# Optimization experiments

Measured on AMD Instinct MI355X. Metric: run time of the kernel, lower is better.

The kernel has to match this reference:

```python
import jax, jax.numpy as jnp
import numpy as np

L, D, V, BS, H, HD, DL = 12, 768, 50257, 1024, 12, 64, 256
B, T = 2, 1024
EPS = 1e-5


def _ln(x, w, b):
    m = jnp.mean(x, axis=-1, keepdims=True)
    v = jnp.mean((x - m) ** 2, axis=-1, keepdims=True)
    return (x - m) * jax.lax.rsqrt(v + EPS) * w + b


def _rope_tables(t_len):
    inv_freq = 1.0 / (10000.0 ** (jnp.arange(0, HD, 2, dtype=jnp.float32) / HD))
    t = jnp.arange(t_len, dtype=jnp.float32)
    freqs = jnp.outer(t, inv_freq)  # [T, HD/2]
    return jnp.cos(freqs), jnp.sin(freqs)


def _apply_rope(x, cos, sin):
    # x: [B, H, T, HD]; cos/sin: [T, HD/2]
    c = jnp.concatenate([cos, cos], axis=-1)[None, None]
    s = jnp.concatenate([sin, sin], axis=-1)[None, None]
    x1, x2 = jnp.split(x, 2, axis=-1)
    rot = jnp.concatenate([-x2, x1], axis=-1)
    return x * c + rot * s


def setup_inputs() -> dict:
    key = jax.random.key(0)
    ks = jax.random.split(key, 16)
    std = 0.02
    n = lambda k, shape: jax.random.normal(k, shape, dtype=jnp.float32) * std
    return {
        'idx': jax.random.randint(ks[0], (B, T), 0, V),
        'wte': n(ks[1], (V, D)),
        'wpe': n(ks[2], (BS, D)),
        'ln1_w': jnp.ones((L, D)), 'ln1_b': jnp.zeros((L, D)),
        'wq_w': n(ks[3], (L, D, H * HD)), 'wq_b': jnp.zeros((L, H * HD)),
        'kva_w': n(ks[4], (L, D, DL)), 'kva_b': jnp.zeros((L, DL)),
        'kvb_w': n(ks[5], (L, DL, 2 * H * HD)), 'kvb_b': jnp.zeros((L, 2 * H * HD)),
        'out_w': n(ks[6], (L, H * HD, D)), 'out_b': jnp.zeros((L, D)),
        'ln2_w': jnp.ones((L, D)), 'ln2_b': jnp.zeros((L, D)),
        'fc_w': n(ks[7], (L, D, 4 * D)), 'fc_b': jnp.zeros((L, 4 * D)),
        'proj_w': n(ks[8], (L, 4 * D, D)), 'proj_b': jnp.zeros((L, D)),
        'lnf_w': jnp.ones((D,)), 'lnf_b': jnp.zeros((D,)),
    }


def _forward(idx, wte, wpe, ln1_w, ln1_b, wq_w, wq_b, kva_w, kva_b, kvb_w, kvb_b,
             out_w, out_b, ln2_w, ln2_b, fc_w, fc_b, proj_w, proj_b, lnf_w, lnf_b):
    b, t = idx.shape
    x = wte[idx] + wpe[:t][None]  # [B,T,D]
    cos, sin = _rope_tables(t)
    scale = 1.0 / np.sqrt(HD)
    causal = jnp.tril(jnp.ones((t, t), dtype=bool))
    for l in range(L):
        h = _ln(x, ln1_w[l], ln1_b[l])
        q = (h @ wq_w[l] + wq_b[l]).reshape(b, t, H, HD).transpose(0, 2, 1, 3)
        kv_latent = h @ kva_w[l] + kva_b[l]  # [B,T,DL] (the cacheable latent)
        kv = (kv_latent @ kvb_w[l] + kvb_b[l]).reshape(b, t, 2, H, HD)
        kv = kv.transpose(2, 0, 3, 1, 4)  # [2,B,H,T,HD]
        k, v = kv[0], kv[1]
        q = _apply_rope(q, cos, sin)
        k = _apply_rope(k, cos, sin)
        scores = jnp.einsum('bhtd,bhsd->bhts', q, k) * scale
        scores = jnp.where(causal[None, None], scores, -jnp.inf)
        probs = jax.nn.softmax(scores, axis=-1)
        attn = jnp.einsum('bhts,bhsd->bhtd', probs, v)
        attn = attn.transpose(0, 2, 1, 3).reshape(b, t, H * HD)
        x = x + attn @ out_w[l] + out_b[l]
        h2 = _ln(x, ln2_w[l], ln2_b[l])
        mlp = jax.nn.gelu(h2 @ fc_w[l] + fc_b[l], approximate=False) @ proj_w[l] + proj_b[l]
        x = x + mlp
    x = _ln(x, lnf_w, lnf_b)
    logits = x @ wte.T  # tied lm_head
    return logits


def reference(idx, wte, wpe, ln1_w, ln1_b, wq_w, wq_b, kva_w, kva_b, kvb_w, kvb_b,
              out_w, out_b, ln2_w, ln2_b, fc_w, fc_b, proj_w, proj_b, lnf_w, lnf_b):
    return _forward(idx, wte, wpe, ln1_w, ln1_b, wq_w, wq_b, kva_w, kva_b, kvb_w,
                    kvb_b, out_w, out_b, ln2_w, ln2_b, fc_w, fc_b, proj_w, proj_b,
                    lnf_w, lnf_b)
```

## Files before the change

kernel.cpp:

```cpp
#include <hip/hip_runtime.h>
#include <cstdint>
#include <cstddef>


typedef unsigned short ushortT;
typedef __bf16 bf16x8 __attribute__((ext_vector_type(8)));
typedef float f32x4 __attribute__((ext_vector_type(4)));

#define NHEAD 12
#define T_SEQ 1024

__device__ __forceinline__ float bf2f(unsigned short u) {
    union { unsigned int i; float f; } v; v.i = ((unsigned int)u) << 16; return v.f;
}
__device__ __forceinline__ unsigned short f2bf(float f) {
    union { float f; unsigned int i; } v; v.f = f;
    unsigned int r = v.i + 0x7fffu + ((v.i >> 16) & 1u);
    return (unsigned short)(r >> 16);
}
__device__ __forceinline__ unsigned int pack2(float a, float b) {
    return (unsigned int)f2bf(a) | ((unsigned int)f2bf(b) << 16);
}
__device__ __forceinline__ void gload_lds16(const void* g, void* l) {
    __builtin_amdgcn_global_load_lds((__attribute__((address_space(1))) void*)g,
                                     (__attribute__((address_space(3))) void*)l, 16, 0, 0);
}
template <int N>
__device__ __forceinline__ void wait_vmcnt() {
    if constexpr (N == 8)      asm volatile("s_waitcnt vmcnt(8)" ::: "memory");
    else if constexpr (N == 6) asm volatile("s_waitcnt vmcnt(6)" ::: "memory");
    else if constexpr (N == 5) asm volatile("s_waitcnt vmcnt(5)" ::: "memory");
    else if constexpr (N == 4) asm volatile("s_waitcnt vmcnt(4)" ::: "memory");
    else if constexpr (N == 3) asm volatile("s_waitcnt vmcnt(3)" ::: "memory");
    else                       asm volatile("s_waitcnt vmcnt(0)" ::: "memory");
}

__global__ __launch_bounds__(256) void transpose_cvt_kernel(
    const float* __restrict__ in, ushortT* __restrict__ outp,
    int K, int N, int outRowOff, size_t outLS) {
    __shared__ float tile[32][33];
    const int tid = threadIdx.x;
    const int n0 = blockIdx.x * 32, k0 = blockIdx.y * 32;
    const float* src = in + (size_t)blockIdx.z * K * N;
    {
        const int r = tid >> 3, cg = tid & 7;
        float4 v = *(const float4*)(src + (size_t)(k0 + r) * N + n0 + cg * 4);
        tile[r][cg * 4 + 0] = v.x; tile[r][cg * 4 + 1] = v.y;
        tile[r][cg * 4 + 2] = v.z; tile[r][cg * 4 + 3] = v.w;
    }
    __syncthreads();
    {
        const int nr = tid >> 3, kg = tid & 7;
        ushort4 o;
        o.x = f2bf(tile[kg * 4 + 0][nr]);
        o.y = f2bf(tile[kg * 4 + 1][nr]);
        o.z = f2bf(tile[kg * 4 + 2][nr]);
        o.w = f2bf(tile[kg * 4 + 3][nr]);
        ushortT* dst = outp + (size_t)blockIdx.z * outLS;
        *(ushort4*)(dst + (size_t)(outRowOff + n0 + nr) * K + k0 + kg * 4) = o;
    }
}

__global__ void cvt_wte_kernel(const float* __restrict__ in, ushortT* __restrict__ outp) {
    size_t i4 = (size_t)blockIdx.x * 256 + threadIdx.x;
    ushort4 o;
    if (i4 < 9649344) {
        float4 v = ((const float4*)in)[i4];
        o.x = f2bf(v.x); o.y = f2bf(v.y); o.z = f2bf(v.z); o.w = f2bf(v.w);
    } else { o.x = 0; o.y = 0; o.z = 0; o.w = 0; }
    ((ushort4*)outp)[i4] = o;
}

__global__ void embed_kernel(const int* __restrict__ idx, const float* __restrict__ wte,
                             const float* __restrict__ wpe, float* __restrict__ x) {
    int i = blockIdx.x * 256 + threadIdx.x;
    int row = i / 768, d = i - row * 768;
    int t = row & 1023;
    x[i] = wte[(size_t)idx[row] * 768 + d] + wpe[(size_t)t * 768 + d];
}

__global__ void rope_tables_kernel(float* __restrict__ cosT, float* __restrict__ sinT) {
    int i = blockIdx.x * 256 + threadIdx.x;
    int t = i >> 5, f = i & 31;
    float invf = exp2f(-(float)f * (13.287712379549449f / 32.0f));
    float ang = (float)t * invf;
    cosT[i] = cosf(ang);
    sinT[i] = sinf(ang);
}

__global__ __launch_bounds__(256) void ln_kernel(const float* __restrict__ x,
                                                 const float* __restrict__ wg,
                                                 const float* __restrict__ bg,
                                                 ushortT* __restrict__ outp) {
    const int row = blockIdx.x, tid = threadIdx.x;
    const float* xr = x + (size_t)row * 768;
    float v0 = xr[tid], v1 = xr[tid + 256], v2 = xr[tid + 512];
    float s = v0 + v1 + v2;
    float ss = v0 * v0 + v1 * v1 + v2 * v2;
#pragma unroll
    for (int off = 32; off >= 1; off >>= 1) {
        s += __shfl_xor(s, off);
        ss += __shfl_xor(ss, off);
    }
    __shared__ float sb[4], ssb[4];
    if ((tid & 63) == 0) { sb[tid >> 6] = s; ssb[tid >> 6] = ss; }
    __syncthreads();
    float S = sb[0] + sb[1] + sb[2] + sb[3];
    float SS = ssb[0] + ssb[1] + ssb[2] + ssb[3];
    const float mean = S * (1.0f / 768.0f);
    float var = SS * (1.0f / 768.0f) - mean * mean;
    const float rs = rsqrtf(var + 1e-5f);
    ushortT* orow = outp + (size_t)row * 768;
    orow[tid]       = f2bf((v0 - mean) * rs * wg[tid]       + bg[tid]);
    orow[tid + 256] = f2bf((v1 - mean) * rs * wg[tid + 256] + bg[tid + 256]);
    orow[tid + 512] = f2bf((v2 - mean) * rs * wg[tid + 512] + bg[tid + 512]);
}

template <int NP>
__global__ __launch_bounds__(256) void reduce_ln_kernel(
    float* __restrict__ x, const float* __restrict__ part,
    const float* __restrict__ bias,
    const float* __restrict__ wg, const float* __restrict__ bg,
    ushortT* __restrict__ outp) {
    const int row = blockIdx.x, tid = threadIdx.x;
    const size_t base = (size_t)row * 768;
    float4 v = {0.f, 0.f, 0.f, 0.f};
    if (tid < 192) {
        v = *(const float4*)(x + base + tid * 4);
        const float4 b4 = *(const float4*)(bias + tid * 4);
        v.x += b4.x; v.y += b4.y; v.z += b4.z; v.w += b4.w;
#pragma unroll
        for (int p = 0; p < NP; ++p) {
            const float4 pv = *(const float4*)(part + (size_t)p * 1572864 + base + tid * 4);
            v.x += pv.x; v.y += pv.y; v.z += pv.z; v.w += pv.w;
        }
        *(float4*)(x + base + tid * 4) = v;
    }
    float s = v.x + v.y + v.z + v.w;
    float ss = v.x * v.x + v.y * v.y + v.z * v.z + v.w * v.w;
#pragma unroll
    for (int off = 32; off >= 1; off >>= 1) {
        s += __shfl_xor(s, off);
        ss += __shfl_xor(ss, off);
    }
    __shared__ float sb[4], ssb[4];
    if ((tid & 63) == 0) { sb[tid >> 6] = s; ssb[tid >> 6] = ss; }
    __syncthreads();
    const float S = sb[0] + sb[1] + sb[2] + sb[3];
    const float SS = ssb[0] + ssb[1] + ssb[2] + ssb[3];
    const float mean = S * (1.0f / 768.0f);
    const float var = SS * (1.0f / 768.0f) - mean * mean;
    const float rs = rsqrtf(var + 1e-5f);
    if (tid < 192) {
        const float4 w4 = *(const float4*)(wg + tid * 4);
        const float4 g4 = *(const float4*)(bg + tid * 4);
        ushort4 o;
        o.x = f2bf((v.x - mean) * rs * w4.x + g4.x);
        o.y = f2bf((v.y - mean) * rs * w4.y + g4.y);
        o.z = f2bf((v.z - mean) * rs * w4.z + g4.z);
        o.w = f2bf((v.w - mean) * rs * w4.w + g4.w);
        *(ushort4*)(outp + base + tid * 4) = o;
    }
}

template <int BM, int NF, int NTHR, bool ROPE, bool PARTIAL = false>
__global__ __launch_bounds__(NTHR) void gemmT(
    const ushortT* __restrict__ A, int lda,
    const ushortT* __restrict__ Bt, int ldb,
    int K, int CS, int Nstore,
    const float* __restrict__ bias0, const float* __restrict__ bias1,
    ushortT* __restrict__ outB0, int ld0,
    ushortT* __restrict__ outB1, int ld1, int mode1,
    const float* __restrict__ resid, float* __restrict__ outF, int ldF,
    int act, const float* __restrict__ cosT, const float* __restrict__ sinT) {
    constexpr int WC = (NTHR == 512) ? 4 : 2;
    constexpr int WMR = BM / 2;
    constexpr int MF = WMR / 16;
    constexpr int NFh = NF / WC;
    constexpr int WNh = NFh * 16;
    constexpr int ABYTES = BM * 128;
    constexpr int BBYTES = NF * 2048;
    constexpr int BUFB = ABYTES + BBYTES;
    constexpr int A_LOADS = (BM * 8) / NTHR;
    constexpr int B_LOADS = (NF * 128) / NTHR;
    constexpr int S = A_LOADS + B_LOADS;
    __shared__ __align__(16) char lds[2 * BUFB];
    const int tid = threadIdx.x;
    const int w = tid >> 6, lane = tid & 63;
    const int wm = w / WC, wn = w % WC;
    const int gx = gridDim.x;
    const int nwg = gx * gridDim.y;
    const int flat = blockIdx.x + gx * blockIdx.y;
    const int xcd = flat & 7, loc = flat >> 3;
    const int qq = nwg >> 3, rr_ = nwg & 7;
    const int swz = (xcd < rr_ ? xcd * (qq + 1) : rr_ * (qq + 1) + (xcd - rr_) * qq) + loc;
    const int m0 = (swz % gx) * BM, n0 = (swz / gx) * NF * 16;
    const int fr = lane & 15, kg = lane >> 4;
    const size_t ldaB = (size_t)lda * 2, ldbB = (size_t)ldb * 2;
    int koff = 0;
    if constexpr (PARTIAL) koff = blockIdx.z * K;
    const char* Ab = (const char*)A + (size_t)koff * 2;
    const char* Bb = (const char*)Bt + (size_t)koff * 2;
    float* outFz = outF;
    if constexpr (PARTIAL) outFz = outF + (size_t)blockIdx.z * 2048 * (size_t)ldF;
    f32x4 acc[MF][NFh] = {};

    auto stage = [&](int buf, int t) {
        const size_t ktB = (size_t)t << 7;
        char* As_ = lds + buf * BUFB;
        char* Bs_ = As_ + ABYTES;
#pragma unroll
        for (int jj = 0; jj < A_LOADS; ++jj) {
            const int i = tid + jj * NTHR;
            const int r = i >> 3, c = i & 7, cc = c ^ (r & 7);
            gload_lds16(Ab + (size_t)(m0 + r) * ldaB + ktB + cc * 16, As_ + i * 16);
        }
#pragma unroll
        for (int jj = 0; jj < B_LOADS; ++jj) {
            const int i = tid + jj * NTHR;
            const int r = i >> 3, c = i & 7, cc = c ^ (r & 7);
            gload_lds16(Bb + (size_t)(n0 + r) * ldbB + ktB + cc * 16, Bs_ + i * 16);
        }
    };

    const int nk = K >> 6;
    stage(0, 0);
    if (nk > 1) { stage(1, 1); wait_vmcnt<S>(); }
    else        { wait_vmcnt<0>(); }
    __builtin_amdgcn_s_barrier();

    for (int t = 0; t < nk; ++t) {
        const int cur = t & 1;
        const char* As_ = lds + cur * BUFB;
        const char* Bs_ = As_ + ABYTES;
        bf16x8 af[MF][2], bfr[NFh][2];
#pragma unroll
        for (int mf = 0; mf < MF; ++mf) {
            const int row = wm * WMR + mf * 16 + fr;
#pragma unroll
            for (int ks = 0; ks < 2; ++ks)
                af[mf][ks] = *(const bf16x8*)(As_ + row * 128 + (((ks * 4 + kg) ^ (row & 7)) << 4));
        }
#pragma unroll
        for (int nf = 0; nf < NFh; ++nf) {
            const int row = wn * WNh + nf * 16 + fr;
#pragma unroll
            for (int ks = 0; ks < 2; ++ks)
                bfr[nf][ks] = *(const bf16x8*)(Bs_ + row * 128 + (((ks * 4 + kg) ^ (row & 7)) << 4));
        }
        if (t + 2 < nk) {
            asm volatile("s_waitcnt lgkmcnt(0)" ::: "memory");
            __builtin_amdgcn_s_barrier();
            stage(cur, t + 2);
        }
#pragma unroll
        for (int ks = 0; ks < 2; ++ks)
#pragma unroll
            for (int nf = 0; nf < NFh; ++nf)
#pragma unroll
                for (int mf = 0; mf < MF; ++mf)
                    acc[mf][nf] = __builtin_amdgcn_mfma_f32_16x16x32_bf16(
                        af[mf][ks], bfr[nf][ks], acc[mf][nf], 0, 0, 0);
        if (t + 1 < nk) {
            if (t + 2 < nk) wait_vmcnt<S>();
            else            wait_vmcnt<0>();
            __builtin_amdgcn_s_barrier();
        }
    }

    if constexpr (ROPE) {
        float vv[MF][4][4];
#pragma unroll
        for (int mf = 0; mf < MF; ++mf)
#pragma unroll
            for (int nf = 0; nf < 4; ++nf) {
                const int gcol = n0 + wn * 64 + nf * 16 + fr;
                float bv = (gcol < CS) ? (bias0 ? bias0[gcol] : 0.0f)
                                       : (bias1 ? bias1[gcol - CS] : 0.0f);
#pragma unroll
                for (int j = 0; j < 4; ++j) vv[mf][nf][j] = acc[mf][nf][j] + bv;
            }
        if (n0 + wn * 64 < 768) {
#pragma unroll
            for (int mf = 0; mf < MF; ++mf)
#pragma unroll
                for (int j = 0; j < 4; ++j) {
                    const int grow = m0 + wm * WMR + mf * 16 + kg * 4 + j;
                    const int t = grow & 1023;
                    const float c0 = cosT[t * 32 + fr],      s0 = sinT[t * 32 + fr];
                    const float c1 = cosT[t * 32 + 16 + fr], s1 = sinT[t * 32 + 16 + fr];
                    float x1 = vv[mf][0][j], x2 = vv[mf][2][j];
                    vv[mf][0][j] = x1 * c0 - x2 * s0;
                    vv[mf][2][j] = x2 * c0 + x1 * s0;
                    float y1 = vv[mf][1][j], y2 = vv[mf][3][j];
                    vv[mf][1][j] = y1 * c1 - y2 * s1;
                    vv[mf][3][j] = y2 * c1 + y1 * s1;
                }
        }
#pragma unroll
        for (int mf = 0; mf < MF; ++mf)
#pragma unroll
            for (int nf = 0; nf < 4; ++nf) {
                const int gcol = n0 + wn * 64 + nf * 16 + fr;
                if (gcol >= Nstore) continue;
#pragma unroll
                for (int j = 0; j < 4; ++j) {
                    const int grow = m0 + wm * WMR + mf * 16 + kg * 4 + j;
                    const float v = vv[mf][nf][j];
                    if (gcol < CS) {
                        if (outB0) outB0[(size_t)grow * ld0 + gcol] = f2bf(v);
                    } else if (outB1) {
                        if (mode1 == 0) {
                            outB1[(size_t)grow * ld1 + gcol - CS] = f2bf(v);
                        } else {
                            const int bb = grow >> 10, tt = grow & 1023;
                            const int hd = gcol - CS;
                            outB1[((size_t)((bb * 12 + (hd >> 6)) * 64 + (hd & 63)) << 10) + tt] = f2bf(v);
                        }
                    }
                }
            }
    } else {
#pragma unroll
        for (int mf = 0; mf < MF; ++mf) {
#pragma unroll
            for (int nf = 0; nf < NFh; ++nf) {
                const int gcol = n0 + wn * WNh + nf * 16 + fr;
                if (gcol >= Nstore) continue;
                float bv = 0.0f;
                if (gcol < CS) { if (bias0) bv = bias0[gcol]; }
                else           { if (bias1) bv = bias1[gcol - CS]; }
#pragma unroll
                for (int j = 0; j < 4; ++j) {
                    const int grow = m0 + wm * WMR + mf * 16 + kg * 4 + j;
                    float v = acc[mf][nf][j] + bv;
                    if (resid) v += resid[(size_t)grow * ldF + gcol];
                    if (act) v = 0.5f * v * (1.0f + erff(v * 0.70710678118654752f));
                    if (outFz) outFz[(size_t)grow * ldF + gcol] = v;
                    if (gcol < CS) {
                        if (outB0) outB0[(size_t)grow * ld0 + gcol] = f2bf(v);
                    } else if (outB1) {
                        if (mode1 == 0) {
                            outB1[(size_t)grow * ld1 + gcol - CS] = f2bf(v);
                        } else {
                            const int bb = grow >> 10, tt = grow & 1023;
                            const int hd = gcol - CS;
                            outB1[((size_t)((bb * 12 + (hd >> 6)) * 64 + (hd & 63)) << 10) + tt] = f2bf(v);
                        }
                    }
                }
            }
        }
    }
}

#define FC_PHASE(SLOT, MB, STAGE_STMT, TAILWAIT)                               \
    {                                                                          \
        bf16x8 af[2][2];                                                       \
        _Pragma("unroll") for (int m = 0; m < 2; ++m)                          \
        _Pragma("unroll") for (int ks = 0; ks < 2; ++ks) {                     \
            const int row = wm * 64 + (MB + m) * 16 + fr;                      \
            af[m][ks] = *(const bf16x8*)(lds + (SLOT) * 16384 + row * 128 +    \
                                         (((ks * 4 + kg) ^ (row & 7)) << 4));  \
        }                                                                      \
        STAGE_STMT;                                                            \
        __builtin_amdgcn_s_barrier();                                          \
        asm volatile("s_waitcnt lgkmcnt(0)" ::: "memory");                     \
        __builtin_amdgcn_sched_barrier(0);                                     \
        __builtin_amdgcn_s_setprio(1);                                         \
        _Pragma("unroll") for (int ks = 0; ks < 2; ++ks)                       \
        _Pragma("unroll") for (int nf = 0; nf < NFW; ++nf)                     \
        _Pragma("unroll") for (int m = 0; m < 2; ++m)                          \
            acc[MB + m][nf] = __builtin_amdgcn_mfma_f32_16x16x32_bf16(         \
                af[m][ks], bfr[nf][ks], acc[MB + m][nf], 0, 0, 0);             \
        __builtin_amdgcn_s_setprio(0);                                         \
        TAILWAIT;                                                              \
        __builtin_amdgcn_s_barrier();                                          \
    }

template <int NFW, bool GELU, bool PARTIAL>
__global__ __launch_bounds__(512, 1) void gemm8(
    const ushortT* __restrict__ A, int lda,
    const ushortT* __restrict__ Bt, int ldb,
    const float* __restrict__ bias,
    ushortT* __restrict__ outB, int ldo,
    float* __restrict__ outF) {
    constexpr int BSLOT = NFW * 8192;
    __shared__ __align__(16) char lds[32768 + 2 * BSLOT];
    const int tid = threadIdx.x;
    const int w = tid >> 6, lane = tid & 63;
    const int wm = w >> 2, wn = w & 3;
    const int fr = lane & 15, kg = lane >> 4;
    const int gx = gridDim.x;
    const int nwg = gx * gridDim.y;
    const int flat = blockIdx.x + gx * blockIdx.y;
    const int cpx = nwg >> 3;
    const int swz = (flat & 7) * cpx + (flat >> 3);
    const int m0 = (swz % gx) * 128, n0 = (swz / gx) * (NFW * 64);
    const size_t ldaB = (size_t)lda * 2, ldbB = (size_t)ldb * 2;
    int koff = 0;
    if constexpr (PARTIAL) koff = blockIdx.z * 768;
    const char* Ag = (const char*)A + (size_t)koff * 2;
    const char* Bg = (const char*)Bt + (size_t)koff * 2;
    float* outFz = nullptr;
    if constexpr (PARTIAL) outFz = outF + (size_t)blockIdx.z * 2048 * 768;

    auto stA = [&](int tile) {
        char* dst = lds + (tile & 1) * 16384;
#pragma unroll
        for (int jj = 0; jj < 2; ++jj) {
            const int i = tid + jj * 512;
            const int r = i >> 3, c = i & 7, cc = c ^ (r & 7);
            gload_lds16(Ag + (size_t)(m0 + r) * ldaB + tile * 128 + cc * 16, dst + i * 16);
        }
    };
    auto stB = [&](int tile) {
        char* dst = lds + 32768 + (tile & 1) * BSLOT;
#pragma unroll
        for (int jj = 0; jj < NFW; ++jj) {
            const int i = tid + jj * 512;
            const int r = i >> 3, c = i & 7, cc = c ^ (r & 7);
            gload_lds16(Bg + (size_t)(n0 + r) * ldbB + tile * 128 + cc * 16, dst + i * 16);
        }
    };

    f32x4 acc[4][NFW] = {};
    stA(0); stB(0); stB(1);
    wait_vmcnt<NFW>();
    __builtin_amdgcn_s_barrier();

    const int browB = wn * (NFW * 16);
    for (int i = 0; i < 6; ++i) {
        const int t1 = 2 * i + 1;
        const bool st = (i < 5);
        bf16x8 bfr[NFW][2];
#pragma unroll
        for (int nf = 0; nf < NFW; ++nf)
#pragma unroll
            for (int ks = 0; ks < 2; ++ks) {
                const int row = browB + nf * 16 + fr;
                bfr[nf][ks] = *(const bf16x8*)(lds + 32768 + 0 * BSLOT + row * 128 +
                                               (((ks * 4 + kg) ^ (row & 7)) << 4));
            }
        FC_PHASE(0, 0, stA(t1), )
        FC_PHASE(0, 2, if (st) stB(t1 + 1),
                 if (st) { wait_vmcnt<NFW>(); } else { wait_vmcnt<0>(); }
                 __builtin_amdgcn_sched_barrier(0))
#pragma unroll
        for (int nf = 0; nf < NFW; ++nf)
#pragma unroll
            for (int ks = 0; ks < 2; ++ks) {
                const int row = browB + nf * 16 + fr;
                bfr[nf][ks] = *(const bf16x8*)(lds + 32768 + 1 * BSLOT + row * 128 +
                                               (((ks * 4 + kg) ^ (row & 7)) << 4));
            }
        FC_PHASE(1, 0, if (st) stA(t1 + 1), )
        FC_PHASE(1, 2, if (st) stB(t1 + 2),
                 if (st) { wait_vmcnt<NFW>(); } else { wait_vmcnt<0>(); }
                 __builtin_amdgcn_sched_barrier(0))
    }

#pragma unroll
    for (int mf = 0; mf < 4; ++mf)
#pragma unroll
        for (int nf = 0; nf < NFW; ++nf) {
            const int col = n0 + wn * (NFW * 16) + nf * 16 + fr;
#pragma unroll
            for (int j = 0; j < 4; ++j) {
                const int row = m0 + wm * 64 + mf * 16 + kg * 4 + j;
                if constexpr (PARTIAL) {
                    outFz[(size_t)row * 768 + col] = acc[mf][nf][j];
                } else {
                    float v = acc[mf][nf][j] + bias[col];
                    if constexpr (GELU)
                        v = 0.5f * v * (1.0f + erff(v * 0.70710678118654752f));
                    outB[(size_t)row * ldo + col] = f2bf(v);
                }
            }
        }
}

#define LM_PHASE(SLOT, MB, STAGE_STMT, TAILWAIT)                              \
    {                                                                          \
        bf16x8 af[2][2];                                                       \
        _Pragma("unroll") for (int m = 0; m < 2; ++m)                          \
        _Pragma("unroll") for (int ks = 0; ks < 2; ++ks) {                     \
            const int row = (MB + m) * 16 + fr;                                \
            af[m][ks] = *(const bf16x8*)(Aw + (SLOT) * 32768 + row * 128 +     \
                                         (((ks * 4 + kg) ^ (row & 7)) << 4));  \
        }                                                                      \
        STAGE_STMT;                                                            \
        __builtin_amdgcn_s_barrier();                                          \
        asm volatile("s_waitcnt lgkmcnt(0)" ::: "memory");                     \
        __builtin_amdgcn_sched_barrier(0);                                     \
        __builtin_amdgcn_s_setprio(1);                                         \
        _Pragma("unroll") for (int ks = 0; ks < 2; ++ks)                       \
        _Pragma("unroll") for (int nf = 0; nf < 4; ++nf)                       \
        _Pragma("unroll") for (int m = 0; m < 2; ++m)                          \
            acc[MB + m][nf] = __builtin_amdgcn_mfma_f32_16x16x32_bf16(         \
                af[m][ks], bfr[nf][ks], acc[MB + m][nf], 0, 0, 0);             \
        __builtin_amdgcn_s_setprio(0);                                         \
        TAILWAIT;                                                              \
        __builtin_amdgcn_s_barrier();                                          \
    }

__global__ __launch_bounds__(512, 1) void lmhead8(
    const ushortT* __restrict__ A, const ushortT* __restrict__ Bt,
    float* __restrict__ outF) {
    __shared__ __align__(16) char lds[131072];
    const int tid = threadIdx.x;
    const int w = tid >> 6, lane = tid & 63;
    const int wm = w >> 2, wn = w & 3;
    const int fr = lane & 15, kg = lane >> 4;
    const int flat = blockIdx.x + 8 * blockIdx.y;
    const int swz = (flat & 7) * 197 + (flat >> 3);
    const int m0 = (swz & 7) * 256, n0 = (swz >> 3) * 256;

    const char* Ag = (const char*)A;
    const char* Bg = (const char*)Bt;
    const char* Aw = lds + wm * 16384;
    const char* Bw = lds + 65536 + (wn >> 1) * 16384;
    const int brow0 = (wn & 1) * 64;

    auto stA = [&](int tile, int half) {
        char* dst = lds + (tile & 1) * 32768 + half * 16384;
#pragma unroll
        for (int jj = 0; jj < 2; ++jj) {
            const int i = tid + jj * 512;
            const int r = i >> 3, c = i & 7, cc = c ^ (r & 7);
            gload_lds16(Ag + (size_t)(m0 + half * 128 + r) * 1536 + tile * 128 + cc * 16,
                        dst + i * 16);
        }
    };
    auto stB = [&](int tile, int half) {
        char* dst = lds + 65536 + (tile & 1) * 32768 + half * 16384;
#pragma unroll
        for (int jj = 0; jj < 2; ++jj) {
            const int i = tid + jj * 512;
            const int r = i >> 3, c = i & 7, cc = c ^ (r & 7);
            gload_lds16(Bg + (size_t)(n0 + half * 128 + r) * 1536 + tile * 128 + cc * 16,
                        dst + i * 16);
        }
    };

    f32x4 acc[8][4] = {};
    stA(0, 0); stA(0, 1); stB(0, 0); stB(0, 1); stB(1, 0); stB(1, 1);
    wait_vmcnt<4>();
    __builtin_amdgcn_s_barrier();

    for (int i = 0; i < 6; ++i) {
        const int t1 = 2 * i + 1;
        const bool st = (i < 5);
        bf16x8 bfr[4][2];
#pragma unroll
        for (int nf = 0; nf < 4; ++nf)
#pragma unroll
            for (int ks = 0; ks < 2; ++ks) {
                const int row = brow0 + nf * 16 + fr;
                bfr[nf][ks] = *(const bf16x8*)(Bw + 0 * 32768 + row * 128 +
                                               (((ks * 4 + kg) ^ (row & 7)) << 4));
            }
        LM_PHASE(0, 0, stA(t1, 0), )
        LM_PHASE(0, 2, stA(t1, 1), )
        LM_PHASE(0, 4, if (st) stB(t1 + 1, 0), )
        LM_PHASE(0, 6, if (st) stB(t1 + 1, 1),
                 if (st) { wait_vmcnt<4>(); } else { wait_vmcnt<0>(); }
                 __builtin_amdgcn_sched_barrier(0))
#pragma unroll
        for (int nf = 0; nf < 4; ++nf)
#pragma unroll
            for (int ks = 0; ks < 2; ++ks) {
                const int row = brow0 + nf * 16 + fr;
                bfr[nf][ks] = *(const bf16x8*)(Bw + 1 * 32768 + row * 128 +
                                               (((ks * 4 + kg) ^ (row & 7)) << 4));
            }
        LM_PHASE(1, 0, if (st) stA(t1 + 1, 0), )
        LM_PHASE(1, 2, if (st) stA(t1 + 1, 1), )
        LM_PHASE(1, 4, if (st) stB(t1 + 2, 0), )
        LM_PHASE(1, 6, if (st) stB(t1 + 2, 1),
                 if (st) { wait_vmcnt<4>(); } else { wait_vmcnt<0>(); }
                 __builtin_amdgcn_sched_barrier(0))
    }

#pragma unroll
    for (int mf = 0; mf < 8; ++mf)
#pragma unroll
        for (int nf = 0; nf < 4; ++nf) {
            const int col = n0 + wn * 64 + nf * 16 + fr;
            if (col < 50257) {
#pragma unroll
                for (int j = 0; j < 4; ++j) {
                    const int row = m0 + wm * 128 + mf * 16 + kg * 4 + j;
                    outF[(size_t)row * 50257 + col] = acc[mf][nf][j];
                }
            }
        }
}

__global__ __launch_bounds__(256) void attn_mfma(const ushortT* __restrict__ q,
                                                 const ushortT* __restrict__ kbuf,
                                                 const ushortT* __restrict__ vT,
                                                 ushortT* __restrict__ attnb) {
    __shared__ __align__(16) char lds[41472];
    const int tid = threadIdx.x, w = tid >> 6, lane = tid & 63;
    const int fr = lane & 15, kg = lane >> 4;
    const int flat = blockIdx.x + 16 * blockIdx.y;
    const int nf2 = (flat & 7) * 48 + (flat >> 3);
    const int bh = nf2 >> 4;
    const int b = bh / NHEAD, h = bh % NHEAD;
    const int qb = (15 - (nf2 & 15)) * 64;
    const int q0 = qb + w * 16;
    const int nst = (qb >> 6) + 1, diag = qb >> 6;

    const ushortT* qrow = q + ((size_t)(b * 1024 + q0 + fr) * 768 + h * 64);
    const bf16x8 qf0 = *(const bf16x8*)(qrow + kg * 8);
    const bf16x8 qf1 = *(const bf16x8*)(qrow + 32 + kg * 8);

    const char* kgb = (const char*)kbuf + ((size_t)(b * 1024) * 768 + h * 64) * 2;
    const char* vgb = (const char*)vT + ((size_t)(b * 12 + h) * 65536) * 2;
    char* Pw = lds + 32768 + w * 2176 + fr * 136;

    auto stage = [&](int buf, int st) {
#pragma unroll
        for (int jj = 0; jj < 2; ++jj) {
            const int i = tid + jj * 256;
            const int r = i >> 3, c = i & 7, cc = c ^ (r & 7);
            gload_lds16(kgb + (size_t)(st * 64 + r) * 1536 + cc * 16, lds + buf * 8192 + i * 16);
            gload_lds16(vgb + (size_t)r * 2048 + st * 128 + cc * 16, lds + 16384 + buf * 8192 + i * 16);
        }
    };

    float m_r = -1e30f, l_r = 0.0f;
    f32x4 o[4] = {};

    stage(0, 0);
    if (nst > 1) stage(1, 1);
    for (int st = 0; st < nst; ++st) {
        const int cur = st & 1;
        if (st + 1 < nst) wait_vmcnt<4>();
        else              wait_vmcnt<0>();
        __builtin_amdgcn_s_barrier();
        const char* Kd = lds + cur * 8192;
        const char* Vd = lds + 16384 + cur * 8192;

        f32x4 sfr[4];
        __builtin_amdgcn_s_setprio(1);
#pragma unroll
        for (int n = 0; n < 4; ++n) {
            const int row = n * 16 + fr;
            bf16x8 k0 = *(const bf16x8*)(Kd + row * 128 + ((kg ^ (row & 7)) << 4));
            bf16x8 k1 = *(const bf16x8*)(Kd + row * 128 + (((4 + kg) ^ (row & 7)) << 4));
            f32x4 sa = {0.0f, 0.0f, 0.0f, 0.0f};
            sa = __builtin_amdgcn_mfma_f32_16x16x32_bf16(k0, qf0, sa, 0, 0, 0);
            sa = __builtin_amdgcn_mfma_f32_16x16x32_bf16(k1, qf1, sa, 0, 0, 0);
            sfr[n] = sa;
        }
        __builtin_amdgcn_s_setprio(0);
        const int qoff = w * 16 + fr;
#pragma unroll
        for (int n = 0; n < 4; ++n)
#pragma unroll
            for (int j = 0; j < 4; ++j) {
                float v = sfr[n][j] * 0.125f;
                if (st == diag && (n * 16 + kg * 4 + j) > qoff) v = -1e30f;
                sfr[n][j] = v;
            }
        float tm = -1e30f;
#pragma unroll
        for (int n = 0; n < 4; ++n)
#pragma unroll
            for (int j = 0; j < 4; ++j) tm = fmaxf(tm, sfr[n][j]);
        tm = fmaxf(tm, __shfl_xor(tm, 16));
        tm = fmaxf(tm, __shfl_xor(tm, 32));
        if (!__all(tm <= m_r + 8.0f)) {
            const float mnew = fmaxf(m_r, tm);
            const float fac = __expf(m_r - mnew);
            m_r = mnew;
            l_r *= fac;
            const float ff0 = __shfl(fac, kg * 4 + 0);
            const float ff1 = __shfl(fac, kg * 4 + 1);
            const float ff2 = __shfl(fac, kg * 4 + 2);
            const float ff3 = __shfl(fac, kg * 4 + 3);
#pragma unroll
            for (int nf = 0; nf < 4; ++nf) {
                o[nf][0] *= ff0; o[nf][1] *= ff1; o[nf][2] *= ff2; o[nf][3] *= ff3;
            }
        }
#pragma unroll
        for (int n = 0; n < 4; ++n) {
            float e0 = __expf(sfr[n][0] - m_r);
            float e1 = __expf(sfr[n][1] - m_r);
            float e2 = __expf(sfr[n][2] - m_r);
            float e3 = __expf(sfr[n][3] - m_r);
            l_r += (e0 + e1) + (e2 + e3);
            uint2 pv;
            pv.x = pack2(e0, e1);
            pv.y = pack2(e2, e3);
            *(uint2*)(Pw + n * 32 + kg * 8) = pv;
        }
        __builtin_amdgcn_s_setprio(1);
#pragma unroll
        for (int ks = 0; ks < 2; ++ks) {
            uint2 a0 = *(const uint2*)(Pw + ks * 64 + kg * 16);
            uint2 a1 = *(const uint2*)(Pw + ks * 64 + kg * 16 + 8);
            union { uint4 u; bf16x8 v; } pa;
            pa.u = make_uint4(a0.x, a0.y, a1.x, a1.y);
#pragma unroll
            for (int nf = 0; nf < 4; ++nf) {
                const int row = nf * 16 + fr;
                bf16x8 vf = *(const bf16x8*)(Vd + row * 128 + (((ks * 4 + kg) ^ (row & 7)) << 4));
                o[nf] = __builtin_amdgcn_mfma_f32_16x16x32_bf16(pa.v, vf, o[nf], 0, 0, 0);
            }
        }
        __builtin_amdgcn_s_setprio(0);
        __builtin_amdgcn_s_barrier();
        if (st + 2 < nst) stage(cur, st + 2);
    }

    l_r += __shfl_xor(l_r, 16);
    l_r += __shfl_xor(l_r, 32);
    const float inv = 1.0f / l_r;
    const float iv0 = __shfl(inv, kg * 4 + 0);
    const float iv1 = __shfl(inv, kg * 4 + 1);
    const float iv2 = __shfl(inv, kg * 4 + 2);
    const float iv3 = __shfl(inv, kg * 4 + 3);
#pragma unroll
    for (int nf = 0; nf < 4; ++nf) {
        const size_t base = (size_t)(b * 1024 + q0) * 768 + h * 64 + nf * 16 + fr;
        attnb[base + (size_t)(kg * 4 + 0) * 768] = f2bf(o[nf][0] * iv0);
        attnb[base + (size_t)(kg * 4 + 1) * 768] = f2bf(o[nf][1] * iv1);
        attnb[base + (size_t)(kg * 4 + 2) * 768] = f2bf(o[nf][2] * iv2);
        attnb[base + (size_t)(kg * 4 + 3) * 768] = f2bf(o[nf][3] * iv3);
    }
}

extern "C" void kernel_launch(void* const* d_in, const int* in_sizes, int n_in,
                              void* d_out, int out_size, void* d_ws, size_t ws_size,
                              hipStream_t stream) {
    (void)in_sizes; (void)n_in; (void)out_size; (void)ws_size;
    const int*   idxp   = (const int*)d_in[0];
    const float* wte    = (const float*)d_in[1];
    const float* wpe    = (const float*)d_in[2];
    const float* ln1_w  = (const float*)d_in[3];
    const float* ln1_b  = (const float*)d_in[4];
    const float* wq_w   = (const float*)d_in[5];
    const float* wq_b   = (const float*)d_in[6];
    const float* kva_w  = (const float*)d_in[7];
    const float* kva_b  = (const float*)d_in[8];
    const float* kvb_w  = (const float*)d_in[9];
    const float* kvb_b  = (const float*)d_in[10];
    const float* out_w  = (const float*)d_in[11];
    const float* out_b  = (const float*)d_in[12];
    const float* ln2_w  = (const float*)d_in[13];
    const float* ln2_b  = (const float*)d_in[14];
    const float* fc_w   = (const float*)d_in[15];
    const float* fc_b   = (const float*)d_in[16];
    const float* proj_w = (const float*)d_in[17];
    const float* proj_b = (const float*)d_in[18];
    const float* lnf_w  = (const float*)d_in[19];
    const float* lnf_b  = (const float*)d_in[20];

    char* ws = (char*)d_ws;
    size_t off = 0;
    auto alloc = [&](size_t bytes) -> char* {
        char* p = ws + off;
        off += (bytes + 255) & ~(size_t)255;
        return p;
    };
    ushortT* wqkvaT = (ushortT*)alloc((size_t)12 * 1024 * 768 * 2);
    ushortT* kvbT   = (ushortT*)alloc((size_t)12 * 1536 * 256 * 2);
    ushortT* outT   = (ushortT*)alloc((size_t)12 * 768 * 768 * 2);
    ushortT* fcT    = (ushortT*)alloc((size_t)12 * 3072 * 768 * 2);
    ushortT* projT  = (ushortT*)alloc((size_t)12 * 768 * 3072 * 2);
    ushortT* wteB   = (ushortT*)alloc((size_t)50432 * 768 * 2);
    float* cosT = (float*)alloc((size_t)1024 * 32 * 4);
    float* sinT = (float*)alloc((size_t)1024 * 32 * 4);
    float*   x     = (float*)alloc((size_t)2048 * 768 * 4);
    ushortT* h     = (ushortT*)alloc((size_t)2048 * 768 * 2);
    ushortT* qbuf  = (ushortT*)alloc((size_t)2048 * 768 * 2);
    ushortT* lat   = (ushortT*)alloc((size_t)2048 * 256 * 2);
    ushortT* kvbuf = (ushortT*)alloc((size_t)2048 * 768 * 2);
    ushortT* vTb   = (ushortT*)alloc((size_t)24 * 64 * 1024 * 2);
    ushortT* attnb = (ushortT*)alloc((size_t)2048 * 768 * 2);
    ushortT* fca   = (ushortT*)alloc((size_t)2048 * 3072 * 2);
    float*   partB = (float*)alloc((size_t)4 * 2048 * 768 * 4);

    transpose_cvt_kernel<<<dim3(24, 24, 12), 256, 0, stream>>>(wq_w,  wqkvaT, 768, 768,  0,   (size_t)1024 * 768);
    transpose_cvt_kernel<<<dim3(8,  24, 12), 256, 0, stream>>>(kva_w, wqkvaT, 768, 256,  768, (size_t)1024 * 768);
    transpose_cvt_kernel<<<dim3(48, 8,  12), 256, 0, stream>>>(kvb_w, kvbT,   256, 1536, 0,   (size_t)1536 * 256);
    transpose_cvt_kernel<<<dim3(24, 24, 12), 256, 0, stream>>>(out_w, outT,   768, 768,  0,   (size_t)768 * 768);
    transpose_cvt_kernel<<<dim3(96, 24, 12), 256, 0, stream>>>(fc_w,  fcT,    768, 3072, 0,   (size_t)3072 * 768);
    transpose_cvt_kernel<<<dim3(24, 96, 12), 256, 0, stream>>>(proj_w, projT, 3072, 768, 0,   (size_t)768 * 3072);
    cvt_wte_kernel<<<37824, 256, 0, stream>>>(wte, wteB);
    rope_tables_kernel<<<128, 256, 0, stream>>>(cosT, sinT);
    embed_kernel<<<6144, 256, 0, stream>>>(idxp, wte, wpe, x);
    ln_kernel<<<2048, 256, 0, stream>>>(x, ln1_w, ln1_b, h);

    for (int l = 0; l < 12; ++l) {
        gemmT<64, 8, 256, true><<<dim3(32, 8), 256, 0, stream>>>(
            h, 768, wqkvaT + (size_t)l * 1024 * 768, 768,
            768, 768, 1024, wq_b + l * 768, kva_b + l * 256,
            qbuf, 768, lat, 256, 0, nullptr, nullptr, 0, 0, cosT, sinT);
        gemmT<64, 8, 256, true><<<dim3(32, 12), 256, 0, stream>>>(
            lat, 256, kvbT + (size_t)l * 1536 * 256, 256,
            256, 768, 1536, kvb_b + l * 1536, kvb_b + l * 1536 + 768,
            kvbuf, 768, vTb, 0, 1, nullptr, nullptr, 0, 0, cosT, sinT);
        attn_mfma<<<dim3(16, 24), 256, 0, stream>>>(qbuf, kvbuf, vTb, attnb);
        gemmT<64, 8, 256, false, true><<<dim3(32, 6, 2), 256, 0, stream>>>(
            attnb, 768, outT + (size_t)l * 768 * 768, 768,
            384, 768, 768, nullptr, nullptr,
            nullptr, 0, nullptr, 0, 0, nullptr, partB, 768, 0, nullptr, nullptr);
        reduce_ln_kernel<2><<<2048, 256, 0, stream>>>(
            x, partB, out_b + l * 768, ln2_w + l * 768, ln2_b + l * 768, h);
        gemm8<3, true, false><<<dim3(16, 16), 512, 0, stream>>>(
            h, 768, fcT + (size_t)l * 3072 * 768, 768,
            fc_b + l * 3072, fca, 3072, nullptr);
        gemm8<3, false, true><<<dim3(16, 4, 4), 512, 0, stream>>>(
            fca, 3072, projT + (size_t)l * 768 * 3072, 3072,
            nullptr, nullptr, 0, partB);
        const float* nw = (l < 11) ? ln1_w + (l + 1) * 768 : lnf_w;
        const float* nb = (l < 11) ? ln1_b + (l + 1) * 768 : lnf_b;
        reduce_ln_kernel<4><<<2048, 256, 0, stream>>>(
            x, partB, proj_b + l * 768, nw, nb, h);
    }
    lmhead8<<<dim3(8, 197), 512, 0, stream>>>(h, wteB, (float*)d_out);
}
```

Before: 1.738 ms.

## Replace LM-head kernel with gemm8 F32 path; fold softmax scale into exp2

Drops the dedicated 256x256-tile lmhead8 kernel and runs the tied LM head through gemm8 with a new F32OUT mode using 128x192 tiles over a 16x262 grid. gemm8's launch bounds move to 2 blocks per CU for all its uses. The attention kernel now folds the 1/sqrt(d) scale and log2(e) into exp2f, applies the causal mask only on the diagonal tile, and raises the lazy-rescale threshold from 8 to 64 in raw-score units. Together these aim to cut LM-head tail and occupancy costs and trim per-element softmax ALU work. The trade-offs are less per-tile reuse in the LM head, possible register pressure from the 2-block bound, and relying on the rescale threshold for numerical safety.

```diff
diff --git a/kernel.cpp b/kernel.cpp
--- a/kernel.cpp
+++ b/kernel.cpp
@@ -378,8 +378,8 @@
         __builtin_amdgcn_s_barrier();                                          \
     }
 
-template <int NFW, bool GELU, bool PARTIAL>
-__global__ __launch_bounds__(512, 1) void gemm8(
+template <int NFW, bool GELU, bool PARTIAL, bool F32OUT = false>
+__global__ __launch_bounds__(512, 2) void gemm8(
     const ushortT* __restrict__ A, int lda,
     const ushortT* __restrict__ Bt, int ldb,
     const float* __restrict__ bias,
@@ -468,130 +468,16 @@
 #pragma unroll
             for (int j = 0; j < 4; ++j) {
                 const int row = m0 + wm * 64 + mf * 16 + kg * 4 + j;
-                if constexpr (PARTIAL) {
+                if constexpr (F32OUT) {
+                    if (col < 50257)
+                        outF[(size_t)row * 50257 + col] = acc[mf][nf][j];
+                } else if constexpr (PARTIAL) {
                     outFz[(size_t)row * 768 + col] = acc[mf][nf][j];
                 } else {
                     float v = acc[mf][nf][j] + bias[col];
                     if constexpr (GELU)
                         v = 0.5f * v * (1.0f + erff(v * 0.70710678118654752f));
                     outB[(size_t)row * ldo + col] = f2bf(v);
-                }
-            }
-        }
-}
-
-#define LM_PHASE(SLOT, MB, STAGE_STMT, TAILWAIT)                              \
-    {                                                                          \
-        bf16x8 af[2][2];                                                       \
-        _Pragma("unroll") for (int m = 0; m < 2; ++m)                          \
-        _Pragma("unroll") for (int ks = 0; ks < 2; ++ks) {                     \
-            const int row = (MB + m) * 16 + fr;                                \
-            af[m][ks] = *(const bf16x8*)(Aw + (SLOT) * 32768 + row * 128 +     \
-                                         (((ks * 4 + kg) ^ (row & 7)) << 4));  \
-        }                                                                      \
-        STAGE_STMT;                                                            \
-        __builtin_amdgcn_s_barrier();                                          \
-        asm volatile("s_waitcnt lgkmcnt(0)" ::: "memory");                     \
-        __builtin_amdgcn_sched_barrier(0);                                     \
-        __builtin_amdgcn_s_setprio(1);                                         \
-        _Pragma("unroll") for (int ks = 0; ks < 2; ++ks)                       \
-        _Pragma("unroll") for (int nf = 0; nf < 4; ++nf)                       \
-        _Pragma("unroll") for (int m = 0; m < 2; ++m)                          \
-            acc[MB + m][nf] = __builtin_amdgcn_mfma_f32_16x16x32_bf16(         \
-                af[m][ks], bfr[nf][ks], acc[MB + m][nf], 0, 0, 0);             \
-        __builtin_amdgcn_s_setprio(0);                                         \
-        TAILWAIT;                                                              \
-        __builtin_amdgcn_s_barrier();                                          \
-    }
-
-__global__ __launch_bounds__(512, 1) void lmhead8(
-    const ushortT* __restrict__ A, const ushortT* __restrict__ Bt,
-    float* __restrict__ outF) {
-    __shared__ __align__(16) char lds[131072];
-    const int tid = threadIdx.x;
-    const int w = tid >> 6, lane = tid & 63;
-    const int wm = w >> 2, wn = w & 3;
-    const int fr = lane & 15, kg = lane >> 4;
-    const int flat = blockIdx.x + 8 * blockIdx.y;
-    const int swz = (flat & 7) * 197 + (flat >> 3);
-    const int m0 = (swz & 7) * 256, n0 = (swz >> 3) * 256;
-
-    const char* Ag = (const char*)A;
-    const char* Bg = (const char*)Bt;
-    const char* Aw = lds + wm * 16384;
-    const char* Bw = lds + 65536 + (wn >> 1) * 16384;
-    const int brow0 = (wn & 1) * 64;
-
-    auto stA = [&](int tile, int half) {
-        char* dst = lds + (tile & 1) * 32768 + half * 16384;
-#pragma unroll
-        for (int jj = 0; jj < 2; ++jj) {
-            const int i = tid + jj * 512;
-            const int r = i >> 3, c = i & 7, cc = c ^ (r & 7);
-            gload_lds16(Ag + (size_t)(m0 + half * 128 + r) * 1536 + tile * 128 + cc * 16,
-                        dst + i * 16);
-        }
-    };
-    auto stB = [&](int tile, int half) {
-        char* dst = lds + 65536 + (tile & 1) * 32768 + half * 16384;
-#pragma unroll
-        for (int jj = 0; jj < 2; ++jj) {
-            const int i = tid + jj * 512;
-            const int r = i >> 3, c = i & 7, cc = c ^ (r & 7);
-            gload_lds16(Bg + (size_t)(n0 + half * 128 + r) * 1536 + tile * 128 + cc * 16,
-                        dst + i * 16);
-        }
-    };
-
-    f32x4 acc[8][4] = {};
-    stA(0, 0); stA(0, 1); stB(0, 0); stB(0, 1); stB(1, 0); stB(1, 1);
-    wait_vmcnt<4>();
-    __builtin_amdgcn_s_barrier();
-
-    for (int i = 0; i < 6; ++i) {
-        const int t1 = 2 * i + 1;
-        const bool st = (i < 5);
-        bf16x8 bfr[4][2];
-#pragma unroll
-        for (int nf = 0; nf < 4; ++nf)
-#pragma unroll
-            for (int ks = 0; ks < 2; ++ks) {
-                const int row = brow0 + nf * 16 + fr;
-                bfr[nf][ks] = *(const bf16x8*)(Bw + 0 * 32768 + row * 128 +
-                                               (((ks * 4 + kg) ^ (row & 7)) << 4));
-            }
-        LM_PHASE(0, 0, stA(t1, 0), )
-        LM_PHASE(0, 2, stA(t1, 1), )
-        LM_PHASE(0, 4, if (st) stB(t1 + 1, 0), )
-        LM_PHASE(0, 6, if (st) stB(t1 + 1, 1),
-                 if (st) { wait_vmcnt<4>(); } else { wait_vmcnt<0>(); }
-                 __builtin_amdgcn_sched_barrier(0))
-#pragma unroll
-        for (int nf = 0; nf < 4; ++nf)
-#pragma unroll
-            for (int ks = 0; ks < 2; ++ks) {
-                const int row = brow0 + nf * 16 + fr;
-                bfr[nf][ks] = *(const bf16x8*)(Bw + 1 * 32768 + row * 128 +
-                                               (((ks * 4 + kg) ^ (row & 7)) << 4));
-            }
-        LM_PHASE(1, 0, if (st) stA(t1 + 1, 0), )
-        LM_PHASE(1, 2, if (st) stA(t1 + 1, 1), )
-        LM_PHASE(1, 4, if (st) stB(t1 + 2, 0), )
-        LM_PHASE(1, 6, if (st) stB(t1 + 2, 1),
-                 if (st) { wait_vmcnt<4>(); } else { wait_vmcnt<0>(); }
-                 __builtin_amdgcn_sched_barrier(0))
-    }
-
-#pragma unroll
-    for (int mf = 0; mf < 8; ++mf)
-#pragma unroll
-        for (int nf = 0; nf < 4; ++nf) {
-            const int col = n0 + wn * 64 + nf * 16 + fr;
-            if (col < 50257) {
-#pragma unroll
-                for (int j = 0; j < 4; ++j) {
-                    const int row = m0 + wm * 128 + mf * 16 + kg * 4 + j;
-                    outF[(size_t)row * 50257 + col] = acc[mf][nf][j];
                 }
             }
         }
@@ -611,6 +497,7 @@
     const int qb = (15 - (nf2 & 15)) * 64;
     const int q0 = qb + w * 16;
     const int nst = (qb >> 6) + 1, diag = qb >> 6;
+    const float SC = 0.125f * 1.44269504088896f;
 
     const ushortT* qrow = q + ((size_t)(b * 1024 + q0 + fr) * 768 + h * 64);
     const bf16x8 qf0 = *(const bf16x8*)(qrow + kg * 8);
@@ -656,15 +543,14 @@
             sfr[n] = sa;
         }
         __builtin_amdgcn_s_setprio(0);
-        const int qoff = w * 16 + fr;
-#pragma unroll
-        for (int n = 0; n < 4; ++n)
-#pragma unroll
-            for (int j = 0; j < 4; ++j) {
-                float v = sfr[n][j] * 0.125f;
-                if (st == diag && (n * 16 + kg * 4 + j) > qoff) v = -1e30f;
-                sfr[n][j] = v;
-            }
+        if (st == diag) {
+            const int qoff = w * 16 + fr;
+#pragma unroll
+            for (int n = 0; n < 4; ++n)
+#pragma unroll
+                for (int j = 0; j < 4; ++j)
+                    if ((n * 16 + kg * 4 + j) > qoff) sfr[n][j] = -1e30f;
+        }
         float tm = -1e30f;
 #pragma unroll
         for (int n = 0; n < 4; ++n)
@@ -672,9 +558,9 @@
             for (int j = 0; j < 4; ++j) tm = fmaxf(tm, sfr[n][j]);
         tm = fmaxf(tm, __shfl_xor(tm, 16));
         tm = fmaxf(tm, __shfl_xor(tm, 32));
-        if (!__all(tm <= m_r + 8.0f)) {
+        if (!__all(tm <= m_r + 64.0f)) {
             const float mnew = fmaxf(m_r, tm);
-            const float fac = __expf(m_r - mnew);
+            const float fac = exp2f((m_r - mnew) * SC);
             m_r = mnew;
             l_r *= fac;
             const float ff0 = __shfl(fac, kg * 4 + 0);
@@ -686,12 +572,13 @@
                 o[nf][0] *= ff0; o[nf][1] *= ff1; o[nf][2] *= ff2; o[nf][3] *= ff3;
             }
         }
+        const float m2 = m_r * SC;
 #pragma unroll
         for (int n = 0; n < 4; ++n) {
-            float e0 = __expf(sfr[n][0] - m_r);
-            float e1 = __expf(sfr[n][1] - m_r);
-            float e2 = __expf(sfr[n][2] - m_r);
-            float e3 = __expf(sfr[n][3] - m_r);
+            float e0 = exp2f(sfr[n][0] * SC - m2);
+            float e1 = exp2f(sfr[n][1] * SC - m2);
+            float e2 = exp2f(sfr[n][2] * SC - m2);
+            float e3 = exp2f(sfr[n][3] * SC - m2);
             l_r += (e0 + e1) + (e2 + e3);
             uint2 pv;
             pv.x = pack2(e0, e1);
@@ -823,5 +710,6 @@
         reduce_ln_kernel<4><<<2048, 256, 0, stream>>>(
             x, partB, proj_b + l * 768, nw, nb, h);
     }
-    lmhead8<<<dim3(8, 197), 512, 0, stream>>>(h, wteB, (float*)d_out);
-}
+    gemm8<3, false, false, true><<<dim3(16, 262), 512, 0, stream>>>(
+        h, 768, wteB, 768, nullptr, nullptr, 0, (float*)d_out);
+}
```

Measured after the change: 1.849 ms. 1.06x slower.
